# Optimization experiments

Measured on AMD Instinct MI355X. Metric: run time of the kernel, lower is better.

Reference implementation:

```python
import jax, jax.numpy as jnp
import numpy as np

BN_EPS = 1e-5

def _gcn_layer(h, src, dst, W, b, Wr, br, gamma, beta):
    # GraphConv norm='none': sum over in-edges of (X W), plus bias, then ReLU
    m = h @ W                                        # [N, out]
    agg = jax.ops.segment_sum(m[src], dst, num_segments=h.shape[0])
    new = jax.nn.relu(agg + b)
    # residual branch: relu(Linear(h))
    res = jax.nn.relu(h @ Wr + br)
    out = new + res
    # BatchNorm1d over node axis (training-mode batch stats, affine)
    mu = out.mean(axis=0)
    var = out.var(axis=0)
    return (out - mu) * jax.lax.rsqrt(var + BN_EPS) * gamma + beta

def setup_inputs() -> dict:
    key = jax.random.key(0)
    ks = jax.random.split(key, 8)
    N, E, D = 100000, 1600000, 128
    s = 1.0 / np.sqrt(D)
    return {
        "h": jax.random.normal(ks[0], (N, D), jnp.float32),
        "src": jax.random.randint(ks[1], (E,), 0, N, jnp.int32),
        "dst": jax.random.randint(ks[2], (E,), 0, N, jnp.int32),
        "W0": jax.random.normal(ks[3], (D, D), jnp.float32) * s,
        "b0": jnp.zeros((D,), jnp.float32),
        "Wr0": jax.random.normal(ks[4], (D, D), jnp.float32) * s,
        "br0": jnp.zeros((D,), jnp.float32),
        "g0": jnp.ones((D,), jnp.float32),
        "be0": jnp.zeros((D,), jnp.float32),
        "W1": jax.random.normal(ks[5], (D, D), jnp.float32) * s,
        "b1": jnp.zeros((D,), jnp.float32),
        "Wr1": jax.random.normal(ks[6], (D, D), jnp.float32) * s,
        "br1": jnp.zeros((D,), jnp.float32),
        "g1": jnp.ones((D,), jnp.float32),
        "be1": jnp.zeros((D,), jnp.float32),
        "batch_size": 100,
    }

def reference(h, src, dst, W0, b0, Wr0, br0, g0, be0, W1, b1, Wr1, br1, g1, be1, batch_size):
    x = _gcn_layer(h, src, dst, W0, b0, Wr0, br0, g0, be0)
    x = _gcn_layer(x, src, dst, W1, b1, Wr1, br1, g1, be1)
    out_feats = x.shape[-1]
    return x.reshape(batch_size, -1, out_feats)
```

## Files before the change

kernel.cpp:

```cpp
#include <hip/hip_runtime.h>
#include <hip/hip_bf16.h>
#include <hip/hip_fp16.h>

#define D 128

typedef _Float16 h8 __attribute__((ext_vector_type(8)));
typedef float f4 __attribute__((ext_vector_type(4)));


__global__ void hist_kernel(const int* __restrict__ dst, int* __restrict__ counts, int E) {
    for (int e = blockIdx.x * blockDim.x + threadIdx.x; e < E; e += gridDim.x * blockDim.x)
        atomicAdd(&counts[dst[e]], 1);
}

__global__ __launch_bounds__(256) void scan_block_sums(const int* __restrict__ counts,
                                                       int* __restrict__ bsums, int N) {
    __shared__ int sdata[256];
    int t = threadIdx.x;
    int idx = blockIdx.x * 256 + t;
    sdata[t] = (idx < N) ? counts[idx] : 0;
    __syncthreads();
    for (int s = 128; s > 0; s >>= 1) {
        if (t < s) sdata[t] += sdata[t + s];
        __syncthreads();
    }
    if (t == 0) bsums[blockIdx.x] = sdata[0];
}

__global__ __launch_bounds__(1024) void scan_single(int* __restrict__ bsums, int nb,
                                                    int* __restrict__ offsets, int N, int E) {
    __shared__ int sdata[1024];
    int t = threadIdx.x;
    int v = (t < nb) ? bsums[t] : 0;
    sdata[t] = v;
    __syncthreads();
    for (int off = 1; off < 1024; off <<= 1) {
        int u = (t >= off) ? sdata[t - off] : 0;
        __syncthreads();
        sdata[t] += u;
        __syncthreads();
    }
    if (t < nb) bsums[t] = sdata[t] - v;
    if (t == 0) offsets[N] = E;
}

__global__ __launch_bounds__(256) void scan_final(const int* __restrict__ counts,
                                                  const int* __restrict__ bprefix,
                                                  int* __restrict__ offsets,
                                                  int* __restrict__ cursor, int N) {
    __shared__ int sdata[256];
    int t = threadIdx.x;
    int idx = blockIdx.x * 256 + t;
    int c = (idx < N) ? counts[idx] : 0;
    sdata[t] = c;
    __syncthreads();
    for (int off = 1; off < 256; off <<= 1) {
        int u = (t >= off) ? sdata[t - off] : 0;
        __syncthreads();
        sdata[t] += u;
        __syncthreads();
    }
    if (idx < N) {
        int v = bprefix[blockIdx.x] + (sdata[t] - c);
        offsets[idx] = v;
        cursor[idx] = v;
    }
}

__global__ void fill_csr(const int* __restrict__ src, const int* __restrict__ dst,
                         int* __restrict__ cursor, int* __restrict__ csr, int E) {
    for (int e = blockIdx.x * blockDim.x + threadIdx.x; e < E; e += gridDim.x * blockDim.x) {
        int d = dst[e];
        int p = atomicAdd(&cursor[d], 1);
        csr[p] = src[e];
    }
}


__global__ __launch_bounds__(256) void convert_f16(const float* __restrict__ in,
                                                   __half* __restrict__ out, int n4) {
    for (int i = blockIdx.x * blockDim.x + threadIdx.x; i < n4; i += gridDim.x * blockDim.x) {
        float4 v = ((const float4*)in)[i];
        __half2 h0 = __floats2half2_rn(v.x, v.y);
        __half2 h1 = __floats2half2_rn(v.z, v.w);
        uint2 u;
        u.x = *reinterpret_cast<uint*>(&h0);
        u.y = *reinterpret_cast<uint*>(&h1);
        ((uint2*)out)[i] = u;
    }
}


__global__ __launch_bounds__(256) void pack_weights(const float* __restrict__ W,
                                                    const float* __restrict__ Wr,
                                                    const float* __restrict__ br_in,
                                                    const float* __restrict__ bn_sc,
                                                    const float* __restrict__ bn_sh,
                                                    __half* __restrict__ Wp,
                                                    float* __restrict__ cadd,
                                                    float* __restrict__ brp) {
    int t = threadIdx.x;
    for (int slot = t; slot < 4096; slot += 256) {
        int lane = slot & 63;
        int kt = (slot >> 6) & 3;
        int jt = (slot >> 8) & 7;
        int mat = slot >> 11;
        const float* Wsel = mat ? Wr : W;
        int j = jt * 16 + (lane & 15);
        int kb = kt * 32 + (lane >> 4) * 8;
        __half tmp[8];
        #pragma unroll
        for (int e = 0; e < 8; ++e) {
            int k = kb + e;
            float w = Wsel[k * D + j];
            if (bn_sc) w *= bn_sc[k];
            tmp[e] = __float2half(w);
        }
        *(uint4*)&Wp[(size_t)slot * 8] = *(const uint4*)tmp;
    }
    if (t < D) {
        float c = 0.f, bb = br_in[t];
        if (bn_sh) {
            for (int k = 0; k < D; ++k) {
                float sh = bn_sh[k];
                c += sh * W[k * D + t];
                bb += sh * Wr[k * D + t];
            }
        }
        cadd[t] = c;
        brp[t] = bb;
    }
}


__global__ __launch_bounds__(256) void gather_sum(const __half* __restrict__ x,
                                                  const int* __restrict__ csr,
                                                  const int* __restrict__ offsets,
                                                  __half* __restrict__ agg, int N) {
    int t = threadIdx.x;
    int wave = t >> 6, lane = t & 63;
    int node = blockIdx.x * 4 + wave;
    if (node >= N) return;
    int e0 = offsets[node], e1 = offsets[node + 1];
    const uint* mp = (const uint*)x;
    float a0 = 0.f, a1 = 0.f, c0 = 0.f, c1 = 0.f;
    int e = e0;
    for (; e + 2 <= e1; e += 2) {
        int s0 = csr[e], s1 = csr[e + 1];
        uint p0 = mp[(size_t)s0 * 64 + lane];
        uint p1 = mp[(size_t)s1 * 64 + lane];
        float2 f0 = __half22float2(*reinterpret_cast<__half2*>(&p0));
        float2 f1 = __half22float2(*reinterpret_cast<__half2*>(&p1));
        a0 += f0.x; a1 += f0.y;
        c0 += f1.x; c1 += f1.y;
    }
    if (e < e1) {
        int s = csr[e];
        uint p = mp[(size_t)s * 64 + lane];
        float2 f = __half22float2(*reinterpret_cast<__half2*>(&p));
        a0 += f.x; a1 += f.y;
    }
    __half2 hv = __floats2half2_rn(a0 + c0, a1 + c1);
    ((uint*)agg)[(size_t)node * 64 + lane] = *reinterpret_cast<uint*>(&hv);
}


template <bool OHALF>
__global__ __launch_bounds__(256) void gemm_fused(const __half* __restrict__ x,
                                                  const __half* __restrict__ agg,
                                                  const __half* __restrict__ Wp,
                                                  const float* __restrict__ cadd,
                                                  const float* __restrict__ brp,
                                                  const float* __restrict__ bvec,
                                                  const int* __restrict__ counts,
                                                  void* __restrict__ outbuf,
                                                  float* __restrict__ stats, int N) {
    __shared__ float sds[4][8][16];
    __shared__ float sdq[4][8][16];
    int wv = threadIdx.x >> 6, lane = threadIdx.x & 63;
    int tilebase = blockIdx.x * 64 + wv * 16;
    int kgrp = lane >> 4, j0 = lane & 15;
    int arow = tilebase + j0;
    bool rowok = arow < N;

    h8 ax0 = 0, ax1 = 0, ax2 = 0, ax3 = 0;
    h8 ag0 = 0, ag1 = 0, ag2 = 0, ag3 = 0;
    if (rowok) {
        const __half* xp = x + (size_t)arow * D + kgrp * 8;
        ax0 = *(const h8*)(xp + 0);
        ax1 = *(const h8*)(xp + 32);
        ax2 = *(const h8*)(xp + 64);
        ax3 = *(const h8*)(xp + 96);
        const __half* ap = agg + (size_t)arow * D + kgrp * 8;
        ag0 = *(const h8*)(ap + 0);
        ag1 = *(const h8*)(ap + 32);
        ag2 = *(const h8*)(ap + 64);
        ag3 = *(const h8*)(ap + 96);
    }

    f4 accm[8], accr[8];
    #pragma unroll
    for (int jt = 0; jt < 8; ++jt) { accm[jt] = 0; accr[jt] = 0; }

    const h8* wp = (const h8*)Wp;
    #pragma unroll
    for (int jt = 0; jt < 8; ++jt) {
        const h8* bm = wp + ((size_t)jt * 4) * 64 + lane;
        const h8* bw = wp + ((size_t)(8 + jt) * 4) * 64 + lane;
        accm[jt] = __builtin_amdgcn_mfma_f32_16x16x32_f16(ag0, bm[0 * 64], accm[jt], 0, 0, 0);
        accm[jt] = __builtin_amdgcn_mfma_f32_16x16x32_f16(ag1, bm[1 * 64], accm[jt], 0, 0, 0);
        accm[jt] = __builtin_amdgcn_mfma_f32_16x16x32_f16(ag2, bm[2 * 64], accm[jt], 0, 0, 0);
        accm[jt] = __builtin_amdgcn_mfma_f32_16x16x32_f16(ag3, bm[3 * 64], accm[jt], 0, 0, 0);
        accr[jt] = __builtin_amdgcn_mfma_f32_16x16x32_f16(ax0, bw[0 * 64], accr[jt], 0, 0, 0);
        accr[jt] = __builtin_amdgcn_mfma_f32_16x16x32_f16(ax1, bw[1 * 64], accr[jt], 0, 0, 0);
        accr[jt] = __builtin_amdgcn_mfma_f32_16x16x32_f16(ax2, bw[2 * 64], accr[jt], 0, 0, 0);
        accr[jt] = __builtin_amdgcn_mfma_f32_16x16x32_f16(ax3, bw[3 * 64], accr[jt], 0, 0, 0);
    }

    int orow0 = tilebase + kgrp * 4;
    float dg[4];
    #pragma unroll
    for (int q = 0; q < 4; ++q) {
        int row = orow0 + q;
        dg[q] = (row < N) ? (float)counts[row] : 0.f;
    }

    float ls[8], lq[8];
    #pragma unroll
    for (int jt = 0; jt < 8; ++jt) {
        int j = jt * 16 + j0;
        float cm = cadd[j];
        float bb = brp[j];
        float bj = bvec[j];
        float s = 0.f, qq = 0.f;
        #pragma unroll
        for (int q = 0; q < 4; ++q) {
            int row = orow0 + q;
            float o = 0.f;
            if (row < N) {
                float nw = fmaxf(accm[jt][q] + dg[q] * cm + bj, 0.f);
                float rs = fmaxf(accr[jt][q] + bb, 0.f);
                o = nw + rs;
                if constexpr (OHALF) {
                    ((__half*)outbuf)[(size_t)row * D + j] = __float2half(o);
                } else {
                    ((float*)outbuf)[(size_t)row * D + j] = o;
                }
            }
            s += o;
            qq += o * o;
        }
        ls[jt] = s;
        lq[jt] = qq;
    }

    #pragma unroll
    for (int jt = 0; jt < 8; ++jt) {
        ls[jt] += __shfl_xor(ls[jt], 16);
        ls[jt] += __shfl_xor(ls[jt], 32);
        lq[jt] += __shfl_xor(lq[jt], 16);
        lq[jt] += __shfl_xor(lq[jt], 32);
    }
    if (lane < 16) {
        #pragma unroll
        for (int jt = 0; jt < 8; ++jt) {
            sds[wv][jt][j0] = ls[jt];
            sdq[wv][jt][j0] = lq[jt];
        }
    }
    __syncthreads();
    int tt = threadIdx.x;
    if (tt < 128) {
        int jj0 = tt & 15, jjt = tt >> 4;
        float s = sds[0][jjt][jj0] + sds[1][jjt][jj0] + sds[2][jjt][jj0] + sds[3][jjt][jj0];
        float q = sdq[0][jjt][jj0] + sdq[1][jjt][jj0] + sdq[2][jjt][jj0] + sdq[3][jjt][jj0];
        int copy = blockIdx.x & 7;
        atomicAdd(&stats[copy * 128 + tt], s);
        atomicAdd(&stats[1024 + copy * 128 + tt], q);
    }
}


__global__ void bn_finalize(float* __restrict__ stats, const float* __restrict__ g,
                            const float* __restrict__ be, float invN) {
    int j = threadIdx.x;
    float s = 0.f, q = 0.f;
    #pragma unroll
    for (int c = 0; c < 8; ++c) {
        s += stats[c * 128 + j];
        q += stats[1024 + c * 128 + j];
    }
    float mu = s * invN;
    float var = q * invN - mu * mu;
    float sc = g[j] * rsqrtf(var + 1e-5f);
    stats[2048 + j] = sc;
    stats[2048 + 128 + j] = be[j] - mu * sc;
}

__global__ __launch_bounds__(256) void bn_apply(float* __restrict__ buf,
                                                const float* __restrict__ stats, int n4) {
    for (int i = blockIdx.x * blockDim.x + threadIdx.x; i < n4; i += gridDim.x * blockDim.x) {
        float4 v = ((const float4*)buf)[i];
        int c0 = (i * 4) & 127;
        float4 sc = *(const float4*)&stats[2048 + c0];
        float4 sh = *(const float4*)&stats[2048 + 128 + c0];
        v.x = v.x * sc.x + sh.x;
        v.y = v.y * sc.y + sh.y;
        v.z = v.z * sc.z + sh.z;
        v.w = v.w * sc.w + sh.w;
        ((float4*)buf)[i] = v;
    }
}


static inline char* align_up(char* p, size_t a) {
    return (char*)(((uintptr_t)p + (a - 1)) & ~(uintptr_t)(a - 1));
}

extern "C" void kernel_launch(void* const* d_in, const int* in_sizes, int n_in,
                              void* d_out, int out_size, void* d_ws, size_t ws_size,
                              hipStream_t stream) {
    const float* h   = (const float*)d_in[0];
    const int*   src = (const int*)d_in[1];
    const int*   dst = (const int*)d_in[2];
    const float* W0  = (const float*)d_in[3];
    const float* b0  = (const float*)d_in[4];
    const float* Wr0 = (const float*)d_in[5];
    const float* br0 = (const float*)d_in[6];
    const float* g0  = (const float*)d_in[7];
    const float* be0 = (const float*)d_in[8];
    const float* W1  = (const float*)d_in[9];
    const float* b1  = (const float*)d_in[10];
    const float* Wr1 = (const float*)d_in[11];
    const float* br1 = (const float*)d_in[12];
    const float* g1  = (const float*)d_in[13];
    const float* be1 = (const float*)d_in[14];

    const int N = in_sizes[0] / D;
    const int E = in_sizes[1];
    float* out = (float*)d_out;

    char* p = (char*)d_ws;
    __half* x0_buf = (__half*)p;              p += (size_t)N * D * sizeof(__half);
    p = align_up(p, 256);
    __half* x1_buf = (__half*)p;              p += (size_t)N * D * sizeof(__half);
    p = align_up(p, 256);
    __half* agg_buf = (__half*)p;             p += (size_t)N * D * sizeof(__half);
    p = align_up(p, 256);
    int* counts  = (int*)p;                   p += (size_t)N * sizeof(int);
    p = align_up(p, 256);
    int* offsets = (int*)p;                   p += (size_t)(N + 1) * sizeof(int);
    p = align_up(p, 256);
    int* cursor  = (int*)p;                   p += (size_t)N * sizeof(int);
    p = align_up(p, 256);
    int* bsums   = (int*)p;                   p += 1024 * sizeof(int);
    p = align_up(p, 256);
    int* csr     = (int*)p;                   p += (size_t)E * sizeof(int);
    p = align_up(p, 256);
    float* stats1 = (float*)p;                p += 2304 * sizeof(float);
    p = align_up(p, 256);
    float* stats2 = (float*)p;                p += 2304 * sizeof(float);
    p = align_up(p, 256);
    __half* Wp0 = (__half*)p;                 p += 32768 * sizeof(__half);
    p = align_up(p, 256);
    __half* Wp1 = (__half*)p;                 p += 32768 * sizeof(__half);
    p = align_up(p, 256);
    float* cadd0 = (float*)p;                 p += D * sizeof(float);
    float* brp0  = (float*)p;                 p += D * sizeof(float);
    float* cadd1 = (float*)p;                 p += D * sizeof(float);
    float* brp1  = (float*)p;                 p += D * sizeof(float);
    (void)ws_size;

    const int nb = (N + 255) / 256;
    const float invN = 1.0f / (float)N;

    convert_f16<<<2048, 256, 0, stream>>>(h, x0_buf, N * D / 4);

    hipMemsetAsync(counts, 0, (size_t)N * sizeof(int), stream);
    hist_kernel<<<2048, 256, 0, stream>>>(dst, counts, E);
    scan_block_sums<<<nb, 256, 0, stream>>>(counts, bsums, N);
    scan_single<<<1, 1024, 0, stream>>>(bsums, nb, offsets, N, E);
    scan_final<<<nb, 256, 0, stream>>>(counts, bsums, offsets, cursor, N);
    fill_csr<<<2048, 256, 0, stream>>>(src, dst, cursor, csr, E);

    const int gemm_grid = (N + 63) / 64;
    const int comb_grid = (N + 3) / 4;
    const int n4 = N * D / 4;

    pack_weights<<<1, 256, 0, stream>>>(W0, Wr0, br0, nullptr, nullptr, Wp0, cadd0, brp0);
    gather_sum<<<comb_grid, 256, 0, stream>>>(x0_buf, csr, offsets, agg_buf, N);
    hipMemsetAsync(stats1, 0, 2048 * sizeof(float), stream);
    gemm_fused<true><<<gemm_grid, 256, 0, stream>>>(x0_buf, agg_buf, Wp0, cadd0, brp0,
                                                    b0, counts, x1_buf, stats1, N);
    bn_finalize<<<1, D, 0, stream>>>(stats1, g0, be0, invN);

    pack_weights<<<1, 256, 0, stream>>>(W1, Wr1, br1, stats1 + 2048, stats1 + 2048 + 128,
                                        Wp1, cadd1, brp1);
    gather_sum<<<comb_grid, 256, 0, stream>>>(x1_buf, csr, offsets, agg_buf, N);
    hipMemsetAsync(stats2, 0, 2048 * sizeof(float), stream);
    gemm_fused<false><<<gemm_grid, 256, 0, stream>>>(x1_buf, agg_buf, Wp1, cadd1, brp1,
                                                     b1, counts, out, stats2, N);
    bn_finalize<<<1, D, 0, stream>>>(stats2, g1, be1, invN);
    bn_apply<<<2048, 256, 0, stream>>>(out, stats2, n4);
}
```

Baseline: 703.9 us.

## Use column-blocked fp16 feature layout and partition graph kernels by node range

Features are now stored in eight column blocks of 16 halves per node, so each block is a contiguous [N,16] array. The gather kernel processes one column block per workgroup, with 8 edges in parallel per wave and a shuffle reduction, to improve cache locality of random row reads. Histogram and CSR fill kernels split the grid into 8 groups, each handling only a dst range, which localizes atomics to cut contention and cache thrashing. The cost is that every group rereads dst, the CSR is read 8 times across the gather blocks, and the blocked-layout reads in the GEMM are strided.

```diff
diff --git a/kernel.cpp b/kernel.cpp
--- a/kernel.cpp
+++ b/kernel.cpp
@@ -8,9 +8,17 @@
 typedef float f4 __attribute__((ext_vector_type(4)));
 
 
-__global__ void hist_kernel(const int* __restrict__ dst, int* __restrict__ counts, int E) {
-    for (int e = blockIdx.x * blockDim.x + threadIdx.x; e < E; e += gridDim.x * blockDim.x)
-        atomicAdd(&counts[dst[e]], 1);
+__global__ __launch_bounds__(256) void hist_x(const int* __restrict__ dst,
+                                              int* __restrict__ counts, int E, int N) {
+    int g = blockIdx.x & 7;
+    int lo = (int)(((long long)N * g) >> 3);
+    int hi = (int)(((long long)N * (g + 1)) >> 3);
+    int tid = (blockIdx.x >> 3) * blockDim.x + threadIdx.x;
+    int stride = (gridDim.x >> 3) * blockDim.x;
+    for (int e = tid; e < E; e += stride) {
+        int d = __builtin_nontemporal_load(&dst[e]);
+        if (d >= lo && d < hi) atomicAdd(&counts[d], 1);
+    }
 }
 
 __global__ __launch_bounds__(256) void scan_block_sums(const int* __restrict__ counts,
@@ -67,26 +75,39 @@
     }
 }
 
-__global__ void fill_csr(const int* __restrict__ src, const int* __restrict__ dst,
-                         int* __restrict__ cursor, int* __restrict__ csr, int E) {
-    for (int e = blockIdx.x * blockDim.x + threadIdx.x; e < E; e += gridDim.x * blockDim.x) {
-        int d = dst[e];
-        int p = atomicAdd(&cursor[d], 1);
-        csr[p] = src[e];
-    }
-}
-
-
-__global__ __launch_bounds__(256) void convert_f16(const float* __restrict__ in,
-                                                   __half* __restrict__ out, int n4) {
-    for (int i = blockIdx.x * blockDim.x + threadIdx.x; i < n4; i += gridDim.x * blockDim.x) {
+__global__ __launch_bounds__(256) void fill_csr_x(const int* __restrict__ src,
+                                                  const int* __restrict__ dst,
+                                                  int* __restrict__ cursor,
+                                                  int* __restrict__ csr, int E, int N) {
+    int g = blockIdx.x & 7;
+    int lo = (int)(((long long)N * g) >> 3);
+    int hi = (int)(((long long)N * (g + 1)) >> 3);
+    int tid = (blockIdx.x >> 3) * blockDim.x + threadIdx.x;
+    int stride = (gridDim.x >> 3) * blockDim.x;
+    for (int e = tid; e < E; e += stride) {
+        int d = __builtin_nontemporal_load(&dst[e]);
+        if (d >= lo && d < hi) {
+            int s = __builtin_nontemporal_load(&src[e]);
+            int p = atomicAdd(&cursor[d], 1);
+            csr[p] = s;
+        }
+    }
+}
+
+
+__global__ __launch_bounds__(256) void convert_f16_blocked(const float* __restrict__ in,
+                                                           __half* __restrict__ out, int N) {
+    int total = N * 32;
+    for (int i = blockIdx.x * blockDim.x + threadIdx.x; i < total; i += gridDim.x * blockDim.x) {
+        int row = i >> 5, col4 = i & 31;
         float4 v = ((const float4*)in)[i];
         __half2 h0 = __floats2half2_rn(v.x, v.y);
         __half2 h1 = __floats2half2_rn(v.z, v.w);
         uint2 u;
         u.x = *reinterpret_cast<uint*>(&h0);
         u.y = *reinterpret_cast<uint*>(&h1);
-        ((uint2*)out)[i] = u;
+        int g = col4 >> 2;
+        ((uint2*)out)[((size_t)g * N + row) * 4 + (col4 & 3)] = u;
     }
 }
 
@@ -133,35 +154,47 @@
 }
 
 
-__global__ __launch_bounds__(256) void gather_sum(const __half* __restrict__ x,
-                                                  const int* __restrict__ csr,
-                                                  const int* __restrict__ offsets,
-                                                  __half* __restrict__ agg, int N) {
-    int t = threadIdx.x;
-    int wave = t >> 6, lane = t & 63;
-    int node = blockIdx.x * 4 + wave;
+__global__ __launch_bounds__(256) void gather_blocked(const __half* __restrict__ xb,
+                                                      const int* __restrict__ csr,
+                                                      const int* __restrict__ offsets,
+                                                      __half* __restrict__ aggb, int N) {
+    int g = blockIdx.x & 7;
+    int chunk = blockIdx.x >> 3;
+    int wave = threadIdx.x >> 6, lane = threadIdx.x & 63;
+    int node = chunk * 4 + wave;
     if (node >= N) return;
     int e0 = offsets[node], e1 = offsets[node + 1];
-    const uint* mp = (const uint*)x;
-    float a0 = 0.f, a1 = 0.f, c0 = 0.f, c1 = 0.f;
-    int e = e0;
-    for (; e + 2 <= e1; e += 2) {
-        int s0 = csr[e], s1 = csr[e + 1];
-        uint p0 = mp[(size_t)s0 * 64 + lane];
-        uint p1 = mp[(size_t)s1 * 64 + lane];
+    int sub = lane >> 3, dw = lane & 7;
+    const uint* xp = (const uint*)xb + (size_t)g * N * 8;
+    float a0 = 0.f, a1 = 0.f, b0 = 0.f, b1 = 0.f;
+    int base = e0;
+    for (; base + 16 <= e1; base += 16) {
+        int s0 = __builtin_nontemporal_load(&csr[base + sub]);
+        int s1 = __builtin_nontemporal_load(&csr[base + 8 + sub]);
+        uint p0 = xp[(size_t)s0 * 8 + dw];
+        uint p1 = xp[(size_t)s1 * 8 + dw];
         float2 f0 = __half22float2(*reinterpret_cast<__half2*>(&p0));
         float2 f1 = __half22float2(*reinterpret_cast<__half2*>(&p1));
         a0 += f0.x; a1 += f0.y;
-        c0 += f1.x; c1 += f1.y;
-    }
-    if (e < e1) {
-        int s = csr[e];
-        uint p = mp[(size_t)s * 64 + lane];
-        float2 f = __half22float2(*reinterpret_cast<__half2*>(&p));
-        a0 += f.x; a1 += f.y;
-    }
-    __half2 hv = __floats2half2_rn(a0 + c0, a1 + c1);
-    ((uint*)agg)[(size_t)node * 64 + lane] = *reinterpret_cast<uint*>(&hv);
+        b0 += f1.x; b1 += f1.y;
+    }
+    for (; base < e1; base += 8) {
+        int ei = base + sub;
+        if (ei < e1) {
+            int s = __builtin_nontemporal_load(&csr[ei]);
+            uint p = xp[(size_t)s * 8 + dw];
+            float2 f = __half22float2(*reinterpret_cast<__half2*>(&p));
+            a0 += f.x; a1 += f.y;
+        }
+    }
+    a0 += b0; a1 += b1;
+    a0 += __shfl_xor(a0, 8);  a1 += __shfl_xor(a1, 8);
+    a0 += __shfl_xor(a0, 16); a1 += __shfl_xor(a1, 16);
+    a0 += __shfl_xor(a0, 32); a1 += __shfl_xor(a1, 32);
+    if (sub == 0) {
+        __half2 hv = __floats2half2_rn(a0, a1);
+        ((uint*)aggb)[((size_t)g * N + node) * 8 + dw] = *reinterpret_cast<uint*>(&hv);
+    }
 }
 
 
@@ -186,16 +219,16 @@
     h8 ax0 = 0, ax1 = 0, ax2 = 0, ax3 = 0;
     h8 ag0 = 0, ag1 = 0, ag2 = 0, ag3 = 0;
     if (rowok) {
-        const __half* xp = x + (size_t)arow * D + kgrp * 8;
-        ax0 = *(const h8*)(xp + 0);
-        ax1 = *(const h8*)(xp + 32);
-        ax2 = *(const h8*)(xp + 64);
-        ax3 = *(const h8*)(xp + 96);
-        const __half* ap = agg + (size_t)arow * D + kgrp * 8;
-        ag0 = *(const h8*)(ap + 0);
-        ag1 = *(const h8*)(ap + 32);
-        ag2 = *(const h8*)(ap + 64);
-        ag3 = *(const h8*)(ap + 96);
+        int gb = kgrp >> 1;
+        int go = (kgrp & 1) * 8;
+        ax0 = *(const h8*)(x + ((size_t)(0 + gb) * N + arow) * 16 + go);
+        ax1 = *(const h8*)(x + ((size_t)(2 + gb) * N + arow) * 16 + go);
+        ax2 = *(const h8*)(x + ((size_t)(4 + gb) * N + arow) * 16 + go);
+        ax3 = *(const h8*)(x + ((size_t)(6 + gb) * N + arow) * 16 + go);
+        ag0 = *(const h8*)(agg + ((size_t)(0 + gb) * N + arow) * 16 + go);
+        ag1 = *(const h8*)(agg + ((size_t)(2 + gb) * N + arow) * 16 + go);
+        ag2 = *(const h8*)(agg + ((size_t)(4 + gb) * N + arow) * 16 + go);
+        ag3 = *(const h8*)(agg + ((size_t)(6 + gb) * N + arow) * 16 + go);
     }
 
     f4 accm[8], accr[8];
@@ -242,7 +275,7 @@
                 float rs = fmaxf(accr[jt][q] + bb, 0.f);
                 o = nw + rs;
                 if constexpr (OHALF) {
-                    ((__half*)outbuf)[(size_t)row * D + j] = __float2half(o);
+                    ((__half*)outbuf)[((size_t)jt * N + row) * 16 + j0] = __float2half(o);
                 } else {
                     ((float*)outbuf)[(size_t)row * D + j] = o;
                 }
@@ -374,21 +407,21 @@
     const int nb = (N + 255) / 256;
     const float invN = 1.0f / (float)N;
 
-    convert_f16<<<2048, 256, 0, stream>>>(h, x0_buf, N * D / 4);
+    convert_f16_blocked<<<2048, 256, 0, stream>>>(h, x0_buf, N);
 
     hipMemsetAsync(counts, 0, (size_t)N * sizeof(int), stream);
-    hist_kernel<<<2048, 256, 0, stream>>>(dst, counts, E);
+    hist_x<<<2048, 256, 0, stream>>>(dst, counts, E, N);
     scan_block_sums<<<nb, 256, 0, stream>>>(counts, bsums, N);
     scan_single<<<1, 1024, 0, stream>>>(bsums, nb, offsets, N, E);
     scan_final<<<nb, 256, 0, stream>>>(counts, bsums, offsets, cursor, N);
-    fill_csr<<<2048, 256, 0, stream>>>(src, dst, cursor, csr, E);
+    fill_csr_x<<<2048, 256, 0, stream>>>(src, dst, cursor, csr, E, N);
 
     const int gemm_grid = (N + 63) / 64;
-    const int comb_grid = (N + 3) / 4;
+    const int gath_grid = 8 * ((N + 3) / 4);
     const int n4 = N * D / 4;
 
     pack_weights<<<1, 256, 0, stream>>>(W0, Wr0, br0, nullptr, nullptr, Wp0, cadd0, brp0);
-    gather_sum<<<comb_grid, 256, 0, stream>>>(x0_buf, csr, offsets, agg_buf, N);
+    gather_blocked<<<gath_grid, 256, 0, stream>>>(x0_buf, csr, offsets, agg_buf, N);
     hipMemsetAsync(stats1, 0, 2048 * sizeof(float), stream);
     gemm_fused<true><<<gemm_grid, 256, 0, stream>>>(x0_buf, agg_buf, Wp0, cadd0, brp0,
                                                     b0, counts, x1_buf, stats1, N);
@@ -396,7 +429,7 @@
 
     pack_weights<<<1, 256, 0, stream>>>(W1, Wr1, br1, stats1 + 2048, stats1 + 2048 + 128,
                                         Wp1, cadd1, brp1);
-    gather_sum<<<comb_grid, 256, 0, stream>>>(x1_buf, csr, offsets, agg_buf, N);
+    gather_blocked<<<gath_grid, 256, 0, stream>>>(x1_buf, csr, offsets, agg_buf, N);
     hipMemsetAsync(stats2, 0, 2048 * sizeof(float), stream);
     gemm_fused<false><<<gemm_grid, 256, 0, stream>>>(x1_buf, agg_buf, Wp1, cadd1, brp1,
                                                      b1, counts, out, stats2, N);
```

Result: slower. 914.8 us (+30.0%).
